# Performance work log

Hardware: AMD Instinct MI355X
Metric: run time of the kernel (lower is better)

The kernel has to match this reference:

```python
import jax, jax.numpy as jnp
import numpy as np

HIDDEN = 1024
INTER = 4096
EPS = 1e-12


def _ste(q, x):
    # straight-through estimator: forward q, backward identity wrt x
    return x + jax.lax.stop_gradient(q - x)


def setup_inputs() -> dict:
    key = jax.random.key(0)
    ks = jax.random.split(key, 4)
    hidden_states = jax.random.normal(ks[0], (4, 2048, INTER), dtype=jnp.float32)
    input_tensor = jax.random.normal(ks[1], (4, 2048, HIDDEN), dtype=jnp.float32)
    W = jax.random.normal(ks[2], (HIDDEN, INTER), dtype=jnp.float32) * 0.02
    b = jnp.zeros((HIDDEN,), dtype=jnp.float32)
    clip_val = jnp.asarray(2.5, dtype=jnp.float32)  # learnable elastic alpha
    gamma = jnp.ones((HIDDEN,), dtype=jnp.float32)
    beta = jnp.zeros((HIDDEN,), dtype=jnp.float32)
    return {"hidden_states": hidden_states, "input_tensor": input_tensor,
            "W": W, "b": b, "clip_val": clip_val, "gamma": gamma, "beta": beta}


def reference(hidden_states, input_tensor, W, b, clip_val, gamma, beta):
    # --- binary weight (BWN): per-output-channel scale = mean(|W|, axis=in) ---
    w_scale = jnp.mean(jnp.abs(W), axis=1, keepdims=True)  # [hidden, 1]
    W_q = _ste(w_scale * jnp.sign(W), W)                    # [hidden, inter]
    # --- elastic signed binary activation: q = alpha * sign(x / alpha) ---
    s = hidden_states / clip_val
    x_q = clip_val * _ste(jnp.sign(s), s)                   # [b, s, inter]
    # --- dense projection ---
    h = jnp.einsum('bsi,hi->bsh', x_q, W_q) + b             # [b, s, hidden]
    # dropout prob 0.0 (eval mode) -> no-op
    # --- residual + LayerNorm (eps=1e-12) ---
    r = h + input_tensor
    mu = jnp.mean(r, axis=-1, keepdims=True)
    var = jnp.mean(jnp.square(r - mu), axis=-1, keepdims=True)
    out = (r - mu) * jax.lax.rsqrt(var + EPS) * gamma + beta
    return out
```

## Files before the change

kernel.cpp:

```cpp
#include <hip/hip_runtime.h>
#include <stdint.h>

#define HIDDEN 1024
#define INTER  4096
#define ROWS   8192
#define BM     32
#define BK     64
#define NKSTEP (INTER / BK)
#define NBLK   (ROWS / BM)
#define BTILE  (HIDDEN * BK)

typedef int i32x4 __attribute__((ext_vector_type(4)));
typedef const uint32_t __attribute__((address_space(1))) gu32;
typedef uint32_t __attribute__((address_space(3))) lu32;

__device__ __forceinline__ uint32_t sgn4(float4 v) {
    uint32_t b0 = (v.x < 0.f) ? 0xFFu : 0x01u;
    uint32_t b1 = (v.y < 0.f) ? 0xFFu : 0x01u;
    uint32_t b2 = (v.z < 0.f) ? 0xFFu : 0x01u;
    uint32_t b3 = (v.w < 0.f) ? 0xFFu : 0x01u;
    return b0 | (b1 << 8) | (b2 << 16) | (b3 << 24);
}

__global__ __launch_bounds__(256)
void pack_w_kernel(const float* __restrict__ W, uint8_t* __restrict__ Bg,
                   float* __restrict__ wscale) {
    int h = blockIdx.x;
    int tid = threadIdx.x;
    int lane = tid & 63, wv = tid >> 6;
    const float4* row = (const float4*)(W + (size_t)h * INTER);
    float asum = 0.f;
    #pragma unroll
    for (int q = 0; q < 4; ++q) {
        int g = q * 256 + tid;
        float4 v = row[g];
        asum += fabsf(v.x) + fabsf(v.y) + fabsf(v.z) + fabsf(v.w);
        int tt = g >> 4;
        *(uint32_t*)(Bg + (size_t)tt * BTILE + h * BK + (g & 15) * 4) = sgn4(v);
    }
    #pragma unroll
    for (int off = 32; off > 0; off >>= 1) asum += __shfl_down(asum, off);
    __shared__ float red[4];
    if (lane == 0) red[wv] = asum;
    __syncthreads();
    if (tid == 0) wscale[h] = (red[0] + red[1] + red[2] + red[3]) * (1.0f / INTER);
}

__global__ __launch_bounds__(512, 2)
void main_kernel(const float* __restrict__ hs, const uint8_t* __restrict__ Bg,
                 const float* __restrict__ wscale, const float* __restrict__ bias,
                 const float* __restrict__ clipp, const float* __restrict__ input,
                 const float* __restrict__ gamma, const float* __restrict__ beta,
                 float* __restrict__ out) {
    __shared__ alignas(16) uint8_t sB[2 * BTILE];
    __shared__ alignas(16) uint8_t sA[2][BM * BK];
    __shared__ float red_s[8][BM], red_q[8][BM];
    __shared__ float s_mu[BM], s_rs[BM];

    const int tid  = threadIdx.x;
    const int lane = tid & 63;
    const int wave = tid >> 6;
    const int m0   = blockIdx.x * BM;

    const int ar = tid >> 4;
    const int ac = tid & 15;
    const int aofs = ar * BK + ac * 4;
    const float* aload_base = hs + (size_t)(m0 + ar) * INTER + ac * 4;

    const int l15 = lane & 15;
    const int kc  = lane >> 4;
    int aro[2], bro[8];
    #pragma unroll
    for (int rt = 0; rt < 2; ++rt) aro[rt] = (rt * 16 + l15) * BK + kc * 16;
    #pragma unroll
    for (int ct = 0; ct < 8; ++ct)
        bro[ct] = (wave * 128 + ct * 16 + l15) * BK + kc * 16;

    i32x4 acc[2][8];
    #pragma unroll
    for (int rt = 0; rt < 2; ++rt)
        #pragma unroll
        for (int ct = 0; ct < 8; ++ct) acc[rt][ct] = (i32x4){0, 0, 0, 0};

    {
        float4 av = *(const float4*)(aload_base);
        const uint8_t* gs = Bg + wave * 8192 + lane * 16;
        uint8_t* ld = &sB[wave * 8192];
        #pragma unroll
        for (int j = 0; j < 8; ++j)
            __builtin_amdgcn_global_load_lds((gu32*)(gs + j * 1024),
                                             (lu32*)(ld + j * 1024), 16, 0, 0);
        *(uint32_t*)&sA[0][aofs] = sgn4(av);
    }
    __syncthreads();

    for (int t = 0; t < NKSTEP; ++t) {
        const int cur = t & 1;
        const int nxt = cur ^ 1;
        const bool more = (t + 1 < NKSTEP);
        float4 av;
        if (more) {
            av = *(const float4*)(aload_base + (t + 1) * BK);
            const uint8_t* gs = Bg + (size_t)(t + 1) * BTILE + wave * 8192 + lane * 16;
            uint8_t* ld = &sB[nxt * BTILE + wave * 8192];
            #pragma unroll
            for (int j = 0; j < 8; ++j)
                __builtin_amdgcn_global_load_lds((gu32*)(gs + j * 1024),
                                                 (lu32*)(ld + j * 1024), 16, 0, 0);
        }
        const uint8_t* bb = &sB[cur * BTILE];
        i32x4 a0 = *(const i32x4*)&sA[cur][aro[0]];
        i32x4 a1 = *(const i32x4*)&sA[cur][aro[1]];
        #pragma unroll
        for (int ct = 0; ct < 8; ++ct) {
            i32x4 bf = *(const i32x4*)&bb[bro[ct]];
            acc[0][ct] = __builtin_amdgcn_mfma_i32_16x16x64_i8(a0, bf, acc[0][ct], 0, 0, 0);
            acc[1][ct] = __builtin_amdgcn_mfma_i32_16x16x64_i8(a1, bf, acc[1][ct], 0, 0, 0);
        }
        if (more) *(uint32_t*)&sA[nxt][aofs] = sgn4(av);
        __syncthreads();
    }

    float clip = clipp[0];
    float cw[8], bi[8];
    const int hb = wave * 128 + l15;
    #pragma unroll
    for (int ct = 0; ct < 8; ++ct) {
        cw[ct] = clip * wscale[hb + ct * 16];
        bi[ct] = bias[hb + ct * 16];
    }
    float* yl = (float*)sB;
    float sp[2][4] = {}, qp[2][4] = {};
    const int rb = (lane >> 4) * 4;
    #pragma unroll
    for (int rt = 0; rt < 2; ++rt) {
        #pragma unroll
        for (int ct = 0; ct < 8; ++ct) {
            int hcol = hb + ct * 16;
            #pragma unroll
            for (int rg = 0; rg < 4; ++rg) {
                int rl = rt * 16 + rb + rg;
                float v = fmaf((float)acc[rt][ct][rg], cw[ct],
                               bi[ct] + input[(size_t)(m0 + rl) * HIDDEN + hcol]);
                sp[rt][rg] += v;
                qp[rt][rg] += v * v;
                yl[rl * HIDDEN + hcol] = v;
            }
        }
    }
    #pragma unroll
    for (int off = 1; off <= 8; off <<= 1) {
        #pragma unroll
        for (int rt = 0; rt < 2; ++rt)
            #pragma unroll
            for (int rg = 0; rg < 4; ++rg) {
                sp[rt][rg] += __shfl_xor(sp[rt][rg], off);
                qp[rt][rg] += __shfl_xor(qp[rt][rg], off);
            }
    }
    if (l15 == 0) {
        int g = lane >> 4;
        #pragma unroll
        for (int rt = 0; rt < 2; ++rt)
            #pragma unroll
            for (int rg = 0; rg < 4; ++rg) {
                red_s[wave][rt * 16 + g * 4 + rg] = sp[rt][rg];
                red_q[wave][rt * 16 + g * 4 + rg] = qp[rt][rg];
            }
    }
    __syncthreads();
    if (tid < BM) {
        float ss = 0.f, qq = 0.f;
        #pragma unroll
        for (int w = 0; w < 8; ++w) { ss += red_s[w][tid]; qq += red_q[w][tid]; }
        float mu  = ss * (1.0f / HIDDEN);
        float var = fmaf(-mu, mu, qq * (1.0f / HIDDEN));
        s_mu[tid] = mu;
        s_rs[tid] = rsqrtf(var + 1e-12f);
    }
    __syncthreads();

    const float4* gmp = (const float4*)gamma;
    const float4* btp = (const float4*)beta;
    const float4* yv  = (const float4*)yl;
    float4* outp = (float4*)(out + (size_t)m0 * HIDDEN);
    #pragma unroll
    for (int j = 0; j < 16; ++j) {
        int f  = j * 512 + tid;
        int rl = f >> 8;
        int c4 = f & 255;
        float4 y4 = yv[f];
        float4 g4 = gmp[c4], b4 = btp[c4];
        float mu = s_mu[rl], rs = s_rs[rl];
        float4 o;
        o.x = (y4.x - mu) * rs * g4.x + b4.x;
        o.y = (y4.y - mu) * rs * g4.y + b4.y;
        o.z = (y4.z - mu) * rs * g4.z + b4.z;
        o.w = (y4.w - mu) * rs * g4.w + b4.w;
        outp[f] = o;
    }
}

extern "C" void kernel_launch(void* const* d_in, const int* in_sizes, int n_in,
                              void* d_out, int out_size, void* d_ws, size_t ws_size,
                              hipStream_t stream) {
    const float* hs    = (const float*)d_in[0];
    const float* inp   = (const float*)d_in[1];
    const float* W     = (const float*)d_in[2];
    const float* b     = (const float*)d_in[3];
    const float* clip  = (const float*)d_in[4];
    const float* gamma = (const float*)d_in[5];
    const float* beta  = (const float*)d_in[6];
    float* out = (float*)d_out;

    uint8_t* Bg   = (uint8_t*)d_ws;
    float* wscale = (float*)((char*)d_ws + (size_t)NKSTEP * BTILE);

    pack_w_kernel<<<HIDDEN, 256, 0, stream>>>(W, Bg, wscale);
    main_kernel<<<NBLK, 512, 0, stream>>>(hs, Bg, wscale, b, clip,
                                          inp, gamma, beta, out);
}
```

Before: 320.5 us.

## Pre-swizzle fragment layouts, prefetch two K-steps ahead, coalesce residual in epilogue

Weights are packed into an MFMA-fragment-ordered layout so each lane reads a contiguous 16-byte fragment from LDS, and activations are written to LDS in the same swizzled order, which is meant to remove bank conflicts. The K loop now issues the global-to-LDS B loads two steps ahead, using explicit vmcnt/lgkmcnt waits and raw barriers instead of __syncthreads, so memory latency overlaps more compute. The epilogue no longer gathers the residual input with scattered per-element loads. It writes the scaled GEMM result to LDS, then adds the input with coalesced float4 row loads and reduces per row with shuffles. The hand-written waitcnt sequencing is fragile and must exactly match the order in which the loads are issued.

```diff
diff --git a/kernel.cpp b/kernel.cpp
--- a/kernel.cpp
+++ b/kernel.cpp
@@ -6,9 +6,9 @@
 #define ROWS   8192
 #define BM     32
 #define BK     64
-#define NKSTEP (INTER / BK)
-#define NBLK   (ROWS / BM)
-#define BTILE  (HIDDEN * BK)
+#define NKSTEP 64
+#define NBLK   256
+#define BTILE  65536
 
 typedef int i32x4 __attribute__((ext_vector_type(4)));
 typedef const uint32_t __attribute__((address_space(1))) gu32;
@@ -29,14 +29,16 @@
     int tid = threadIdx.x;
     int lane = tid & 63, wv = tid >> 6;
     const float4* row = (const float4*)(W + (size_t)h * INTER);
+    const uint32_t base_h = (uint32_t)(h >> 4) * 1024u + (uint32_t)(h & 15) * 16u;
     float asum = 0.f;
     #pragma unroll
     for (int q = 0; q < 4; ++q) {
         int g = q * 256 + tid;
         float4 v = row[g];
         asum += fabsf(v.x) + fabsf(v.y) + fabsf(v.z) + fabsf(v.w);
-        int tt = g >> 4;
-        *(uint32_t*)(Bg + (size_t)tt * BTILE + h * BK + (g & 15) * 4) = sgn4(v);
+        uint32_t off = (uint32_t)(g >> 4) * (uint32_t)BTILE + base_h
+                     + (uint32_t)((g & 15) >> 2) * 256u + (uint32_t)(g & 3) * 4u;
+        *(uint32_t*)(Bg + off) = sgn4(v);
     }
     #pragma unroll
     for (int off = 32; off > 0; off >>= 1) asum += __shfl_down(asum, off);
@@ -53,8 +55,7 @@
                  const float* __restrict__ gamma, const float* __restrict__ beta,
                  float* __restrict__ out) {
     __shared__ alignas(16) uint8_t sB[2 * BTILE];
-    __shared__ alignas(16) uint8_t sA[2][BM * BK];
-    __shared__ float red_s[8][BM], red_q[8][BM];
+    __shared__ alignas(16) uint8_t sA[2 * 2048];
     __shared__ float s_mu[BM], s_rs[BM];
 
     const int tid  = threadIdx.x;
@@ -64,124 +65,119 @@
 
     const int ar = tid >> 4;
     const int ac = tid & 15;
-    const int aofs = ar * BK + ac * 4;
-    const float* aload_base = hs + (size_t)(m0 + ar) * INTER + ac * 4;
-
+    const int awofs = (ar >> 4) * 1024 + ((ac >> 2) * 16 + (ar & 15)) * 16 + (ac & 3) * 4;
+    const float* aload = hs + (size_t)(m0 + ar) * INTER + ac * 4;
+
+    const uint8_t* bsrc = Bg + wave * 8192 + lane * 16;
+    uint8_t* bdst0 = sB + wave * 8192;
+    const int fofs = lane * 16;
+
+    i32x4 acc0[8], acc1[8];
+    #pragma unroll
+    for (int ct = 0; ct < 8; ++ct) {
+        acc0[ct] = (i32x4){0, 0, 0, 0};
+        acc1[ct] = (i32x4){0, 0, 0, 0};
+    }
+
+    float4 av0 = *(const float4*)(aload);
+    #pragma unroll
+    for (int j = 0; j < 8; ++j)
+        __builtin_amdgcn_global_load_lds((gu32*)(bsrc + j * 1024),
+                                         (lu32*)(bdst0 + j * 1024), 16, 0, 0);
+    float4 av1 = *(const float4*)(aload + 64);
+    #pragma unroll
+    for (int j = 0; j < 8; ++j)
+        __builtin_amdgcn_global_load_lds((gu32*)(bsrc + BTILE + j * 1024),
+                                         (lu32*)(bdst0 + BTILE + j * 1024), 16, 0, 0);
+    *(uint32_t*)&sA[awofs] = sgn4(av0);
+    asm volatile("s_waitcnt lgkmcnt(0)" ::: "memory");
+    __builtin_amdgcn_s_barrier();
+
+#define GEMM_BODY(T, CUR, DO_WRITE, DO_ISSUE, VM, AVW, AVL) do {              \
+    asm volatile("s_waitcnt vmcnt(" #VM ")" ::: "memory");                    \
+    const uint8_t* bb_ = sB + (CUR) * BTILE + wave * 8192;                    \
+    i32x4 a0_ = *(const i32x4*)&sA[(CUR) * 2048 + fofs];                      \
+    i32x4 a1_ = *(const i32x4*)&sA[(CUR) * 2048 + 1024 + fofs];               \
+    _Pragma("unroll")                                                         \
+    for (int ct_ = 0; ct_ < 8; ++ct_) {                                       \
+        i32x4 bf_ = *(const i32x4*)&bb_[ct_ * 1024 + fofs];                   \
+        acc0[ct_] = __builtin_amdgcn_mfma_i32_16x16x64_i8(a0_, bf_, acc0[ct_], 0, 0, 0); \
+        acc1[ct_] = __builtin_amdgcn_mfma_i32_16x16x64_i8(a1_, bf_, acc1[ct_], 0, 0, 0); \
+    }                                                                         \
+    if (DO_WRITE) *(uint32_t*)&sA[((CUR) ^ 1) * 2048 + awofs] = sgn4(AVW);    \
+    asm volatile("s_waitcnt lgkmcnt(0)" ::: "memory");                        \
+    if (DO_ISSUE) {                                                           \
+        AVL = *(const float4*)(aload + ((T) + 2) * 64);                       \
+        _Pragma("unroll")                                                     \
+        for (int j_ = 0; j_ < 8; ++j_)                                        \
+            __builtin_amdgcn_global_load_lds(                                 \
+                (gu32*)(bsrc + (size_t)((T) + 2) * BTILE + j_ * 1024),        \
+                (lu32*)(bdst0 + (CUR) * BTILE + j_ * 1024), 16, 0, 0);        \
+    }                                                                         \
+    __builtin_amdgcn_s_barrier();                                             \
+} while (0)
+
+    for (int tt = 0; tt < 31; ++tt) {
+        const int t0 = 2 * tt;
+        GEMM_BODY(t0,     0, 1, 1, 9, av1, av0);
+        GEMM_BODY(t0 + 1, 1, 1, 1, 9, av0, av1);
+    }
+    GEMM_BODY(62, 0, 1, 0, 9, av1, av0);
+    GEMM_BODY(63, 1, 0, 0, 0, av0, av0);
+#undef GEMM_BODY
+
+    float clip = clipp[0];
     const int l15 = lane & 15;
-    const int kc  = lane >> 4;
-    int aro[2], bro[8];
-    #pragma unroll
-    for (int rt = 0; rt < 2; ++rt) aro[rt] = (rt * 16 + l15) * BK + kc * 16;
-    #pragma unroll
-    for (int ct = 0; ct < 8; ++ct)
-        bro[ct] = (wave * 128 + ct * 16 + l15) * BK + kc * 16;
-
-    i32x4 acc[2][8];
-    #pragma unroll
-    for (int rt = 0; rt < 2; ++rt)
-        #pragma unroll
-        for (int ct = 0; ct < 8; ++ct) acc[rt][ct] = (i32x4){0, 0, 0, 0};
-
-    {
-        float4 av = *(const float4*)(aload_base);
-        const uint8_t* gs = Bg + wave * 8192 + lane * 16;
-        uint8_t* ld = &sB[wave * 8192];
-        #pragma unroll
-        for (int j = 0; j < 8; ++j)
-            __builtin_amdgcn_global_load_lds((gu32*)(gs + j * 1024),
-                                             (lu32*)(ld + j * 1024), 16, 0, 0);
-        *(uint32_t*)&sA[0][aofs] = sgn4(av);
-    }
-    __syncthreads();
-
-    for (int t = 0; t < NKSTEP; ++t) {
-        const int cur = t & 1;
-        const int nxt = cur ^ 1;
-        const bool more = (t + 1 < NKSTEP);
-        float4 av;
-        if (more) {
-            av = *(const float4*)(aload_base + (t + 1) * BK);
-            const uint8_t* gs = Bg + (size_t)(t + 1) * BTILE + wave * 8192 + lane * 16;
-            uint8_t* ld = &sB[nxt * BTILE + wave * 8192];
-            #pragma unroll
-            for (int j = 0; j < 8; ++j)
-                __builtin_amdgcn_global_load_lds((gu32*)(gs + j * 1024),
-                                                 (lu32*)(ld + j * 1024), 16, 0, 0);
-        }
-        const uint8_t* bb = &sB[cur * BTILE];
-        i32x4 a0 = *(const i32x4*)&sA[cur][aro[0]];
-        i32x4 a1 = *(const i32x4*)&sA[cur][aro[1]];
-        #pragma unroll
-        for (int ct = 0; ct < 8; ++ct) {
-            i32x4 bf = *(const i32x4*)&bb[bro[ct]];
-            acc[0][ct] = __builtin_amdgcn_mfma_i32_16x16x64_i8(a0, bf, acc[0][ct], 0, 0, 0);
-            acc[1][ct] = __builtin_amdgcn_mfma_i32_16x16x64_i8(a1, bf, acc[1][ct], 0, 0, 0);
-        }
-        if (more) *(uint32_t*)&sA[nxt][aofs] = sgn4(av);
-        __syncthreads();
-    }
-
-    float clip = clipp[0];
+    const int hb  = wave * 128 + l15;
+    const int rb  = (lane >> 4) * 4;
     float cw[8], bi[8];
-    const int hb = wave * 128 + l15;
     #pragma unroll
     for (int ct = 0; ct < 8; ++ct) {
         cw[ct] = clip * wscale[hb + ct * 16];
         bi[ct] = bias[hb + ct * 16];
     }
+
     float* yl = (float*)sB;
-    float sp[2][4] = {}, qp[2][4] = {};
-    const int rb = (lane >> 4) * 4;
-    #pragma unroll
-    for (int rt = 0; rt < 2; ++rt) {
+    #pragma unroll
+    for (int ct = 0; ct < 8; ++ct) {
         #pragma unroll
-        for (int ct = 0; ct < 8; ++ct) {
-            int hcol = hb + ct * 16;
-            #pragma unroll
-            for (int rg = 0; rg < 4; ++rg) {
-                int rl = rt * 16 + rb + rg;
-                float v = fmaf((float)acc[rt][ct][rg], cw[ct],
-                               bi[ct] + input[(size_t)(m0 + rl) * HIDDEN + hcol]);
-                sp[rt][rg] += v;
-                qp[rt][rg] += v * v;
-                yl[rl * HIDDEN + hcol] = v;
-            }
+        for (int rg = 0; rg < 4; ++rg) {
+            yl[(rb + rg) * HIDDEN + hb + ct * 16]      = fmaf((float)acc0[ct][rg], cw[ct], bi[ct]);
+            yl[(16 + rb + rg) * HIDDEN + hb + ct * 16] = fmaf((float)acc1[ct][rg], cw[ct], bi[ct]);
         }
     }
+    __syncthreads();
+
+    const int erow = tid >> 4;
+    const int ecol = tid & 15;
+    const float4* in4 = (const float4*)(input + (size_t)(m0 + erow) * HIDDEN);
+    float4* ylr = (float4*)(yl + erow * HIDDEN);
+    float s = 0.f, q = 0.f;
+    #pragma unroll
+    for (int i = 0; i < 16; ++i) {
+        int f = ecol + i * 16;
+        float4 y4 = ylr[f];
+        float4 r4 = in4[f];
+        y4.x += r4.x; y4.y += r4.y; y4.z += r4.z; y4.w += r4.w;
+        s += y4.x + y4.y + y4.z + y4.w;
+        q += y4.x * y4.x + y4.y * y4.y + y4.z * y4.z + y4.w * y4.w;
+        ylr[f] = y4;
+    }
     #pragma unroll
     for (int off = 1; off <= 8; off <<= 1) {
-        #pragma unroll
-        for (int rt = 0; rt < 2; ++rt)
-            #pragma unroll
-            for (int rg = 0; rg < 4; ++rg) {
-                sp[rt][rg] += __shfl_xor(sp[rt][rg], off);
-                qp[rt][rg] += __shfl_xor(qp[rt][rg], off);
-            }
-    }
-    if (l15 == 0) {
-        int g = lane >> 4;
-        #pragma unroll
-        for (int rt = 0; rt < 2; ++rt)
-            #pragma unroll
-            for (int rg = 0; rg < 4; ++rg) {
-                red_s[wave][rt * 16 + g * 4 + rg] = sp[rt][rg];
-                red_q[wave][rt * 16 + g * 4 + rg] = qp[rt][rg];
-            }
+        s += __shfl_xor(s, off);
+        q += __shfl_xor(q, off);
+    }
+    if (ecol == 0) {
+        float mu  = s * (1.0f / HIDDEN);
+        float var = fmaf(-mu, mu, q * (1.0f / HIDDEN));
+        s_mu[erow] = mu;
+        s_rs[erow] = rsqrtf(var + 1e-12f);
     }
     __syncthreads();
-    if (tid < BM) {
-        float ss = 0.f, qq = 0.f;
-        #pragma unroll
-        for (int w = 0; w < 8; ++w) { ss += red_s[w][tid]; qq += red_q[w][tid]; }
-        float mu  = ss * (1.0f / HIDDEN);
-        float var = fmaf(-mu, mu, qq * (1.0f / HIDDEN));
-        s_mu[tid] = mu;
-        s_rs[tid] = rsqrtf(var + 1e-12f);
-    }
-    __syncthreads();
-
-    const float4* gmp = (const float4*)gamma;
-    const float4* btp = (const float4*)beta;
+
+    const float4* gm4 = (const float4*)gamma;
+    const float4* bt4 = (const float4*)beta;
     const float4* yv  = (const float4*)yl;
     float4* outp = (float4*)(out + (size_t)m0 * HIDDEN);
     #pragma unroll
@@ -190,7 +186,7 @@
         int rl = f >> 8;
         int c4 = f & 255;
         float4 y4 = yv[f];
-        float4 g4 = gmp[c4], b4 = btp[c4];
+        float4 g4 = gm4[c4], b4 = bt4[c4];
         float mu = s_mu[rl], rs = s_rs[rl];
         float4 o;
         o.x = (y4.x - mu) * rs * g4.x + b4.x;
```

After: 295.4 us. -7.8%, faster.
